# Kernel tuning notes

Hardware: AMD Instinct MI355X
Metric: run time of the kernel (lower is better)

## Reference

```python
import jax, jax.numpy as jnp
import numpy as np

N = 8192
IN_FEATS = 512
OUT_FEATS = 64
ALPHA = 0.2  # LeakyReLU negative slope
NEG_INF = -9e15


def setup_inputs() -> dict:
    key = jax.random.key(0)
    k_h, k_adj, k_W, k_a = jax.random.split(key, 4)
    h = jax.random.normal(k_h, (N, IN_FEATS), dtype=jnp.float32)
    adj = (jax.random.uniform(k_adj, (N, N)) < 0.01).astype(jnp.float32)
    adj = jnp.maximum(adj, jnp.eye(N, dtype=jnp.float32))
    # xavier_uniform with gain=1.414
    def xavier(k, shape, gain=1.414):
        limit = gain * np.sqrt(6.0 / (shape[0] + shape[1]))
        return jax.random.uniform(k, shape, minval=-limit, maxval=limit, dtype=jnp.float32)
    W = xavier(k_W, (IN_FEATS, OUT_FEATS))
    a = xavier(k_a, (2 * OUT_FEATS, 1))
    return {"h": h, "adj": adj, "W": W, "a": a}


def reference(h, adj, W, a):
    Wh = h @ W  # [N, F]
    # Decompose e_ij = LeakyReLU(a1 . Wh_i + a2 . Wh_j) -- same math as the
    # repeat+cat formulation, without the [N, N, 2F] intermediate.
    a1 = a[:OUT_FEATS, 0]   # [F]
    a2 = a[OUT_FEATS:, 0]   # [F]
    f1 = Wh @ a1            # [N]
    f2 = Wh @ a2            # [N]
    e = jax.nn.leaky_relu(f1[:, None] + f2[None, :], negative_slope=ALPHA)  # [N, N]
    e = jnp.where(adj > 0, e, NEG_INF)
    attention = jax.nn.softmax(e, axis=1)
    # dropout is identity in eval mode (training=False)
    h_prime = attention @ Wh  # [N, F]
    return jax.nn.elu(h_prime)  # concat=True
```

## Files before the change

kernel.cpp:

```cpp
#include <hip/hip_runtime.h>
#include <hip/hip_bf16.h>

#define NN 8192
#define INF_ 512
#define OUTF 64
#define ALPHA_ 0.2f
#define CAPR 192
#define NWORDS 256
#define ABLKS (NN / 8)
#define SBLKS (NN / 2)

using f32x4 = __attribute__((ext_vector_type(4))) float;

__device__ inline unsigned short f2bf(float x) {
    __hip_bfloat16 b = __float2bfloat16(x);
    return *reinterpret_cast<unsigned short*>(&b);
}
__device__ inline float bf2f(unsigned short u) {
    const unsigned int v = (unsigned int)u << 16;
    return __builtin_bit_cast(float, v);
}

__global__ __launch_bounds__(256) void gat_scan_wh_kernel(
    const float* __restrict__ adj, const float* __restrict__ h,
    const float* __restrict__ W, const float* __restrict__ a,
    unsigned int* __restrict__ g_mask, unsigned short* __restrict__ WhB,
    float* __restrict__ f1, float* __restrict__ f2)
{
    const int t = threadIdx.x;

    if (blockIdx.x < ABLKS) {
        __shared__ float red[4][8][64];
        const int l = t & 63;
        const int w = __builtin_amdgcn_readfirstlane(t >> 6);
        const int row0 = blockIdx.x * 8;

        const float* hb = h + (size_t)row0 * INF_ + w * 128;

        float acc[8];
        #pragma unroll
        for (int r = 0; r < 8; ++r) acc[r] = 0.f;

        for (int k0 = 0; k0 < 128; k0 += 4) {
            f32x4 hv[8];
            #pragma unroll
            for (int r = 0; r < 8; ++r)
                hv[r] = *(const f32x4*)(hb + r * INF_ + k0);
            #pragma unroll
            for (int kk = 0; kk < 4; ++kk) {
                const float wv = W[(w * 128 + k0 + kk) * OUTF + l];
                #pragma unroll
                for (int r = 0; r < 8; ++r)
                    acc[r] += hv[r][kk] * wv;
            }
        }
        #pragma unroll
        for (int r = 0; r < 8; ++r) red[w][r][l] = acc[r];
        __syncthreads();

        if (t < 64) {
            const float a1 = a[t], a2 = a[64 + t];
            #pragma unroll
            for (int r = 0; r < 8; ++r) {
                const float wh = red[0][r][t] + red[1][r][t] + red[2][r][t] + red[3][r][t];
                WhB[(size_t)(row0 + r) * OUTF + t] = f2bf(wh);
                float v1 = wh * a1;
                float v2 = wh * a2;
                #pragma unroll
                for (int m = 32; m >= 1; m >>= 1) {
                    v1 += __shfl_xor(v1, m, 64);
                    v2 += __shfl_xor(v2, m, 64);
                }
                if (t == 0) { f1[row0 + r] = v1; f2[row0 + r] = v2; }
            }
        }
        return;
    }

    const int row0 = (blockIdx.x - ABLKS) * 2;

    f32x4 v0[8], v1[8];
    {
        const f32x4* r0p = (const f32x4*)(adj + (size_t)row0 * NN);
        const f32x4* r1p = (const f32x4*)(adj + (size_t)(row0 + 1) * NN);
        #pragma unroll
        for (int q = 0; q < 8; ++q) v0[q] = __builtin_nontemporal_load(&r0p[t + q * 256]);
        #pragma unroll
        for (int q = 0; q < 8; ++q) v1[q] = __builtin_nontemporal_load(&r1p[t + q * 256]);
    }

    unsigned int m0 = 0, m1 = 0;
    #pragma unroll
    for (int q = 0; q < 8; ++q) {
        const unsigned int n0 = (v0[q][0] > 0.f ? 1u : 0u) | (v0[q][1] > 0.f ? 2u : 0u)
                              | (v0[q][2] > 0.f ? 4u : 0u) | (v0[q][3] > 0.f ? 8u : 0u);
        const unsigned int n1 = (v1[q][0] > 0.f ? 1u : 0u) | (v1[q][1] > 0.f ? 2u : 0u)
                              | (v1[q][2] > 0.f ? 4u : 0u) | (v1[q][3] > 0.f ? 8u : 0u);
        m0 |= n0 << (4 * q);
        m1 |= n1 << (4 * q);
    }
    g_mask[(size_t)row0 * NWORDS + t]       = m0;
    g_mask[(size_t)(row0 + 1) * NWORDS + t] = m1;
}

__global__ __launch_bounds__(256) void gat_out_kernel(
    const unsigned int* __restrict__ g_mask,
    const float* __restrict__ f1, const float* __restrict__ f2,
    const unsigned short* __restrict__ WhB, float* __restrict__ out)
{
    __shared__ int   s_e[4][CAPR];
    __shared__ float s_p[4][CAPR];

    const int t = threadIdx.x;
    const int w = t >> 6, l = t & 63;
    const int row = blockIdx.x * 4 + w;

    const uint4 mv = *(const uint4*)(g_mask + (size_t)row * NWORDS + 4 * l);
    const int c = __popc(mv.x) + __popc(mv.y) + __popc(mv.z) + __popc(mv.w);

    int inc = c;
    #pragma unroll
    for (int d = 1; d < 64; d <<= 1) {
        const int v = __shfl_up(inc, d, 64);
        if (l >= d) inc += v;
    }
    int o = inc - c;
    int cnt = __shfl(inc, 63, 64);
    cnt = cnt < CAPR ? cnt : CAPR;

    const unsigned int wd_[4] = {mv.x, mv.y, mv.z, mv.w};
    #pragma unroll
    for (int k = 0; k < 4; ++k) {
        unsigned int wd = wd_[k];
        const int pos4 = 4 * (4 * l + k);
        while (wd) {
            const int b = __ffs(wd) - 1;
            wd &= wd - 1;
            const int col = pos4 + ((b >> 2) << 10) + (b & 3);
            if (o < CAPR) s_e[w][o] = col;
            ++o;
        }
    }
    __syncthreads();

    const float f1i = f1[row];
    for (int e = l; e < cnt; e += 64) {
        float x = f1i + f2[s_e[w][e]];
        x = x > 0.f ? x : ALPHA_ * x;
        s_p[w][e] = __expf(x);
    }
    __syncthreads();

    float acc = 0.f, ps = 0.f;
    int e = 0;
    for (; e + 7 < cnt; e += 8) {
        int jj[8]; float pp[8], gg[8];
        #pragma unroll
        for (int k = 0; k < 8; ++k) { jj[k] = s_e[w][e + k]; pp[k] = s_p[w][e + k]; }
        #pragma unroll
        for (int k = 0; k < 8; ++k) gg[k] = bf2f(WhB[(size_t)jj[k] * OUTF + l]);
        #pragma unroll
        for (int k = 0; k < 8; ++k) { ps += pp[k]; acc += pp[k] * gg[k]; }
    }
    for (; e < cnt; ++e) {
        const int j0 = s_e[w][e];
        const float p0 = s_p[w][e];
        ps  += p0;
        acc += p0 * bf2f(WhB[(size_t)j0 * OUTF + l]);
    }

    const float hp = acc / ps;
    out[(size_t)row * OUTF + l] = hp > 0.f ? hp : (__expf(hp) - 1.f);
}

extern "C" void kernel_launch(void* const* d_in, const int* in_sizes, int n_in,
                              void* d_out, int out_size, void* d_ws, size_t ws_size,
                              hipStream_t stream) {
    const float* h   = (const float*)d_in[0];
    const float* adj = (const float*)d_in[1];
    const float* W   = (const float*)d_in[2];
    const float* a   = (const float*)d_in[3];
    float* out = (float*)d_out;

    unsigned short* WhB    = (unsigned short*)d_ws;
    float*          f1     = (float*)(WhB + (size_t)NN * OUTF);
    float*          f2     = f1 + NN;
    unsigned int*   g_mask = (unsigned int*)(f2 + NN);

    gat_scan_wh_kernel<<<ABLKS + SBLKS, 256, 0, stream>>>(adj, h, W, a, g_mask, WhB, f1, f2);
    gat_out_kernel    <<<NN / 4,        256, 0, stream>>>(g_mask, f1, f2, WhB, out);
}
```

Baseline: 65.97 us.

## Split each output row across two wavefronts in the aggregation kernel

The gather/aggregate kernel now assigns two wavefronts per row instead of one. The mask scan, the exp computation and the neighbor accumulation are split across both halves. Partial sums are combined through shared memory. This doubles the block count and shortens the per-wave serial gather latency chain, at the cost of extra syncthreads and shared-memory reductions. The total run time is likely dominated by the adj-scan kernel, which reads the 256MB adjacency matrix.

```diff
diff --git a/kernel.cpp b/kernel.cpp
--- a/kernel.cpp
+++ b/kernel.cpp
@@ -108,15 +108,21 @@
     const float* __restrict__ f1, const float* __restrict__ f2,
     const unsigned short* __restrict__ WhB, float* __restrict__ out)
 {
-    __shared__ int   s_e[4][CAPR];
-    __shared__ float s_p[4][CAPR];
+    __shared__ int   s_e[2][CAPR];
+    __shared__ float s_p[2][CAPR];
+    __shared__ float s_acc[2][64];
+    __shared__ float s_ps[2];
+    __shared__ int   s_half[2][2];
 
     const int t = threadIdx.x;
     const int w = t >> 6, l = t & 63;
-    const int row = blockIdx.x * 4 + w;
-
-    const uint4 mv = *(const uint4*)(g_mask + (size_t)row * NWORDS + 4 * l);
-    const int c = __popc(mv.x) + __popc(mv.y) + __popc(mv.z) + __popc(mv.w);
+    const int r = w >> 1;
+    const int u = w & 1;
+    const int row = blockIdx.x * 2 + r;
+
+    const int wbase = 2 * (u * 64 + l);
+    const uint2 mv = *(const uint2*)(g_mask + (size_t)row * NWORDS + wbase);
+    const int c = __popc(mv.x) + __popc(mv.y);
 
     int inc = c;
     #pragma unroll
@@ -124,53 +130,72 @@
         const int v = __shfl_up(inc, d, 64);
         if (l >= d) inc += v;
     }
-    int o = inc - c;
-    int cnt = __shfl(inc, 63, 64);
+    if (l == 63) s_half[r][u] = inc;
+    __syncthreads();
+
+    const int base = u ? s_half[r][0] : 0;
+    int cnt = s_half[r][0] + s_half[r][1];
     cnt = cnt < CAPR ? cnt : CAPR;
-
-    const unsigned int wd_[4] = {mv.x, mv.y, mv.z, mv.w};
+    int o = base + inc - c;
+
+    const unsigned int wd_[2] = {mv.x, mv.y};
     #pragma unroll
-    for (int k = 0; k < 4; ++k) {
+    for (int k = 0; k < 2; ++k) {
         unsigned int wd = wd_[k];
-        const int pos4 = 4 * (4 * l + k);
+        const int pos4 = 4 * (wbase + k);
         while (wd) {
             const int b = __ffs(wd) - 1;
             wd &= wd - 1;
             const int col = pos4 + ((b >> 2) << 10) + (b & 3);
-            if (o < CAPR) s_e[w][o] = col;
+            if (o < CAPR) s_e[r][o] = col;
             ++o;
         }
     }
     __syncthreads();
 
     const float f1i = f1[row];
-    for (int e = l; e < cnt; e += 64) {
-        float x = f1i + f2[s_e[w][e]];
+    for (int e = u * 64 + l; e < cnt; e += 128) {
+        float x = f1i + f2[s_e[r][e]];
         x = x > 0.f ? x : ALPHA_ * x;
-        s_p[w][e] = __expf(x);
-    }
-    __syncthreads();
+        s_p[r][e] = __expf(x);
+    }
+    __syncthreads();
+
+    int h = ((cnt >> 1) + 7) & ~7;
+    if (h > cnt) h = cnt;
+    const int e_lo = u ? h : 0;
+    const int e_hi = u ? cnt : h;
 
     float acc = 0.f, ps = 0.f;
-    int e = 0;
-    for (; e + 7 < cnt; e += 8) {
+    int e = e_lo;
+    for (; e + 7 < e_hi; e += 8) {
         int jj[8]; float pp[8], gg[8];
         #pragma unroll
-        for (int k = 0; k < 8; ++k) { jj[k] = s_e[w][e + k]; pp[k] = s_p[w][e + k]; }
+        for (int k = 0; k < 8; ++k) { jj[k] = s_e[r][e + k]; pp[k] = s_p[r][e + k]; }
         #pragma unroll
         for (int k = 0; k < 8; ++k) gg[k] = bf2f(WhB[(size_t)jj[k] * OUTF + l]);
         #pragma unroll
         for (int k = 0; k < 8; ++k) { ps += pp[k]; acc += pp[k] * gg[k]; }
     }
-    for (; e < cnt; ++e) {
-        const int j0 = s_e[w][e];
-        const float p0 = s_p[w][e];
+    for (; e < e_hi; ++e) {
+        const int j0 = s_e[r][e];
+        const float p0 = s_p[r][e];
         ps  += p0;
         acc += p0 * bf2f(WhB[(size_t)j0 * OUTF + l]);
     }
 
-    const float hp = acc / ps;
-    out[(size_t)row * OUTF + l] = hp > 0.f ? hp : (__expf(hp) - 1.f);
+    if (u == 1) {
+        s_acc[r][l] = acc;
+        if (l == 0) s_ps[r] = ps;
+    }
+    __syncthreads();
+
+    if (u == 0) {
+        acc += s_acc[r][l];
+        ps  += s_ps[r];
+        const float hp = acc / ps;
+        out[(size_t)row * OUTF + l] = hp > 0.f ? hp : (__expf(hp) - 1.f);
+    }
 }
 
 extern "C" void kernel_launch(void* const* d_in, const int* in_sizes, int n_in,
@@ -188,5 +213,5 @@
     unsigned int*   g_mask = (unsigned int*)(f2 + NN);
 
     gat_scan_wh_kernel<<<ABLKS + SBLKS, 256, 0, stream>>>(adj, h, W, a, g_mask, WhB, f1, f2);
-    gat_out_kernel    <<<NN / 4,        256, 0, stream>>>(g_mask, f1, f2, WhB, out);
-}
+    gat_out_kernel    <<<NN / 2,        256, 0, stream>>>(g_mask, f1, f2, WhB, out);
+}
```

Measured after the change: 67.12 us. About the same (+1.8%).

## Compute Wh with bf16 MFMA in a separate kernel from adjacency scan

Applied to the files above, without the earlier changes.

Moves the h@W projection out of the fused scan kernel into its own kernel that stages W in LDS as bf16 and uses 16x16x32 bf16 MFMA instructions, computing f1/f2 with in-wave shuffles. The adjacency bitmask scan becomes a standalone kernel, so there are three launches. This removes the FP32 scalar FMA loop and the LDS cross-wave reduction. In exchange, h is rounded to bf16 before the matmul, which lowers the precision of Wh, f1 and f2, and it adds one kernel launch and loses the overlap between projection and scan blocks.

```diff
diff --git a/kernel.cpp b/kernel.cpp
--- a/kernel.cpp
+++ b/kernel.cpp
@@ -7,10 +7,10 @@
 #define ALPHA_ 0.2f
 #define CAPR 192
 #define NWORDS 256
-#define ABLKS (NN / 8)
 #define SBLKS (NN / 2)
 
-using f32x4 = __attribute__((ext_vector_type(4))) float;
+using f32x4  = __attribute__((ext_vector_type(4))) float;
+using bf16x8 = __attribute__((ext_vector_type(8))) short;
 
 __device__ inline unsigned short f2bf(float x) {
     __hip_bfloat16 b = __float2bfloat16(x);
@@ -21,63 +21,76 @@
     return __builtin_bit_cast(float, v);
 }
 
-__global__ __launch_bounds__(256) void gat_scan_wh_kernel(
-    const float* __restrict__ adj, const float* __restrict__ h,
-    const float* __restrict__ W, const float* __restrict__ a,
-    unsigned int* __restrict__ g_mask, unsigned short* __restrict__ WhB,
+__global__ __launch_bounds__(256) void gat_wh_mfma(
+    const float* __restrict__ h, const float* __restrict__ W,
+    const float* __restrict__ a, unsigned short* __restrict__ WhB,
     float* __restrict__ f1, float* __restrict__ f2)
 {
+    __shared__ unsigned short Wl[INF_ / 8][OUTF][8];
+
     const int t = threadIdx.x;
-
-    if (blockIdx.x < ABLKS) {
-        __shared__ float red[4][8][64];
-        const int l = t & 63;
-        const int w = __builtin_amdgcn_readfirstlane(t >> 6);
-        const int row0 = blockIdx.x * 8;
-
-        const float* hb = h + (size_t)row0 * INF_ + w * 128;
-
-        float acc[8];
-        #pragma unroll
-        for (int r = 0; r < 8; ++r) acc[r] = 0.f;
-
-        for (int k0 = 0; k0 < 128; k0 += 4) {
-            f32x4 hv[8];
-            #pragma unroll
-            for (int r = 0; r < 8; ++r)
-                hv[r] = *(const f32x4*)(hb + r * INF_ + k0);
-            #pragma unroll
-            for (int kk = 0; kk < 4; ++kk) {
-                const float wv = W[(w * 128 + k0 + kk) * OUTF + l];
-                #pragma unroll
-                for (int r = 0; r < 8; ++r)
-                    acc[r] += hv[r][kk] * wv;
-            }
+    for (int i = t; i < INF_ * OUTF; i += 256) {
+        const int k = i >> 6, c = i & 63;
+        Wl[k >> 3][c][k & 7] = f2bf(W[i]);
+    }
+    __syncthreads();
+
+    const int w  = t >> 6, l = t & 63;
+    const int lr = l & 15, lg = l >> 4;
+    const int r0 = blockIdx.x * 64 + w * 16;
+
+    f32x4 acc0 = {0.f,0.f,0.f,0.f}, acc1 = acc0, acc2 = acc0, acc3 = acc0;
+
+    for (int ks = 0; ks < INF_ / 32; ++ks) {
+        const float* hp = h + (size_t)(r0 + lr) * INF_ + ks * 32 + lg * 8;
+        const f32x4 h0 = *(const f32x4*)hp;
+        const f32x4 h1 = *(const f32x4*)(hp + 4);
+        bf16x8 af;
+        #pragma unroll
+        for (int j = 0; j < 4; ++j) {
+            af[j]     = (short)f2bf(h0[j]);
+            af[4 + j] = (short)f2bf(h1[j]);
         }
-        #pragma unroll
-        for (int r = 0; r < 8; ++r) red[w][r][l] = acc[r];
-        __syncthreads();
-
-        if (t < 64) {
-            const float a1 = a[t], a2 = a[64 + t];
-            #pragma unroll
-            for (int r = 0; r < 8; ++r) {
-                const float wh = red[0][r][t] + red[1][r][t] + red[2][r][t] + red[3][r][t];
-                WhB[(size_t)(row0 + r) * OUTF + t] = f2bf(wh);
-                float v1 = wh * a1;
-                float v2 = wh * a2;
-                #pragma unroll
-                for (int m = 32; m >= 1; m >>= 1) {
-                    v1 += __shfl_xor(v1, m, 64);
-                    v2 += __shfl_xor(v2, m, 64);
-                }
-                if (t == 0) { f1[row0 + r] = v1; f2[row0 + r] = v2; }
-            }
+        const int kb = ks * 4 + lg;
+        const bf16x8 b0 = *(const bf16x8*)&Wl[kb][ 0 + lr][0];
+        const bf16x8 b1 = *(const bf16x8*)&Wl[kb][16 + lr][0];
+        const bf16x8 b2 = *(const bf16x8*)&Wl[kb][32 + lr][0];
+        const bf16x8 b3 = *(const bf16x8*)&Wl[kb][48 + lr][0];
+
+        acc0 = __builtin_amdgcn_mfma_f32_16x16x32_bf16(af, b0, acc0, 0, 0, 0);
+        acc1 = __builtin_amdgcn_mfma_f32_16x16x32_bf16(af, b1, acc1, 0, 0, 0);
+        acc2 = __builtin_amdgcn_mfma_f32_16x16x32_bf16(af, b2, acc2, 0, 0, 0);
+        acc3 = __builtin_amdgcn_mfma_f32_16x16x32_bf16(af, b3, acc3, 0, 0, 0);
+    }
+
+    const float a10 = a[lr], a11 = a[16 + lr], a12 = a[32 + lr], a13 = a[48 + lr];
+    const float a20 = a[64 + lr], a21 = a[80 + lr], a22 = a[96 + lr], a23 = a[112 + lr];
+
+    #pragma unroll
+    for (int j = 0; j < 4; ++j) {
+        const int row = r0 + lg * 4 + j;
+        unsigned short* wp = WhB + (size_t)row * OUTF;
+        wp[ 0 + lr] = f2bf(acc0[j]);
+        wp[16 + lr] = f2bf(acc1[j]);
+        wp[32 + lr] = f2bf(acc2[j]);
+        wp[48 + lr] = f2bf(acc3[j]);
+
+        float v1 = acc0[j] * a10 + acc1[j] * a11 + acc2[j] * a12 + acc3[j] * a13;
+        float v2 = acc0[j] * a20 + acc1[j] * a21 + acc2[j] * a22 + acc3[j] * a23;
+        #pragma unroll
+        for (int m = 1; m <= 8; m <<= 1) {
+            v1 += __shfl_xor(v1, m, 64);
+            v2 += __shfl_xor(v2, m, 64);
         }
-        return;
-    }
-
-    const int row0 = (blockIdx.x - ABLKS) * 2;
+        if (lr == 0) { f1[row] = v1; f2[row] = v2; }
+    }
+}
+
+__global__ __launch_bounds__(256) void gat_scan_kernel(
+    const float* __restrict__ adj, unsigned int* __restrict__ g_mask)
+{
+    const int t = threadIdx.x;
+    const int row0 = blockIdx.x * 2;
 
     f32x4 v0[8], v1[8];
     {
@@ -187,6 +200,7 @@
     float*          f2     = f1 + NN;
     unsigned int*   g_mask = (unsigned int*)(f2 + NN);
 
-    gat_scan_wh_kernel<<<ABLKS + SBLKS, 256, 0, stream>>>(adj, h, W, a, g_mask, WhB, f1, f2);
-    gat_out_kernel    <<<NN / 4,        256, 0, stream>>>(g_mask, f1, f2, WhB, out);
-}
+    gat_wh_mfma    <<<NN / 64, 256, 0, stream>>>(h, W, a, WhB, f1, f2);
+    gat_scan_kernel<<<SBLKS,   256, 0, stream>>>(adj, g_mask);
+    gat_out_kernel <<<NN / 4,  256, 0, stream>>>(g_mask, f1, f2, WhB, out);
+}
```

Result: slower. 81.19 us (+23.1%).
